# Performance work log

Measured on AMD Instinct MI355X. Metric: run time of the kernel, lower is better.

The kernel has to match this reference:

```python
import jax, jax.numpy as jnp
import numpy as np
from jax import lax

B, N = 8, 4096
H = 128          # cfg.net.num_hidden
K = 64           # max_num_neighbors
R1, R2 = 0.2, 0.4
S1, S2 = N // 2, N // 8   # sampling ratios 0.5 and 0.25
OUT = 40


def setup_inputs() -> dict:
    key = jax.random.key(0)
    ks = jax.random.split(key, 32)
    inp = {}
    inp["x"] = jax.random.normal(ks[30], (B, N, 3), jnp.float32)
    inp["pos"] = jax.random.uniform(ks[31], (B, N, 3), jnp.float32)  # unit cube -> radii 0.2/0.4 meaningful
    layers = [("sa1_w1", "sa1_b1", 6, H // 2), ("sa1_w2", "sa1_b2", H // 2, H),
              ("sa2_w1", "sa2_b1", H + 3, H), ("sa2_w2", "sa2_b2", H, 2 * H),
              ("sa3_w1", "sa3_b1", 2 * H + 3, 2 * H), ("sa3_w2", "sa3_b2", 2 * H, 4 * H),
              ("sa3_w3", "sa3_b3", 4 * H, 8 * H),
              ("hd_w1", "hd_b1", 8 * H, 4 * H), ("hd_w2", "hd_b2", 4 * H, 2 * H),
              ("hd_w3", "hd_b3", 2 * H, OUT)]
    for i, (wn, bn, fi, fo) in enumerate(layers):
        inp[wn] = jax.random.normal(ks[i], (fi, fo), jnp.float32) / np.sqrt(fi)
        inp[bn] = jnp.zeros((fo,), jnp.float32)
    return inp


def _mlp(h, layers):
    # Linear+ReLU stack, plain last layer (PyG MLP plain_last=True, eval-mode BN is identity)
    n = len(layers)
    for i, (w, b) in enumerate(layers):
        h = h @ w + b
        if i < n - 1:
            h = jax.nn.relu(h)
    return h


def _fps(p, n_samples):
    # farthest point sampling on one cloud p: [N,3] -> [n_samples] int32
    Np = p.shape[0]

    def step(carry, _):
        min_d, last = carry
        d = jnp.sum((p - p[last]) ** 2, -1)
        min_d = jnp.minimum(min_d, d)
        return (min_d, jnp.argmax(min_d).astype(jnp.int32)), last

    _, idxs = lax.scan(step, (jnp.full((Np,), jnp.inf, p.dtype), jnp.int32(0)),
                       None, length=n_samples)
    return idxs


def _sa(xc, pc, n_samples, r, layers):
    # one SA layer on one cloud: xc [N,C], pc [N,3]
    idx = _fps(pc, n_samples)
    c = pc[idx]                                            # [S,3] centers
    d2 = jnp.sum((c[:, None, :] - pc[None, :, :]) ** 2, -1)  # [S,N]
    d2 = jnp.where(d2 <= r * r, d2, jnp.inf)               # ball query mask
    negd, nbr = lax.top_k(-d2, K)                          # K nearest inside ball
    valid = jnp.isfinite(negd)                             # [S,K]
    feat = jnp.concatenate([xc[nbr], pc[nbr] - c[:, None, :]], -1)  # [S,K,C+3]
    h = _mlp(feat, layers)                                 # [S,K,Cout]
    h = jnp.where(valid[..., None], h, -jnp.inf)
    return jnp.max(h, axis=1), c                           # max-pool over neighborhood


def reference(x, pos, sa1_w1, sa1_b1, sa1_w2, sa1_b2,
              sa2_w1, sa2_b1, sa2_w2, sa2_b2,
              sa3_w1, sa3_b1, sa3_w2, sa3_b2, sa3_w3, sa3_b3,
              hd_w1, hd_b1, hd_w2, hd_b2, hd_w3, hd_b3):
    x1, p1 = jax.vmap(lambda xc, pc: _sa(xc, pc, S1, R1,
                                         [(sa1_w1, sa1_b1), (sa1_w2, sa1_b2)]))(x, pos)
    x2, p2 = jax.vmap(lambda xc, pc: _sa(xc, pc, S2, R2,
                                         [(sa2_w1, sa2_b1), (sa2_w2, sa2_b2)]))(x1, p1)
    # GlobalSAModule: MLP(cat([x,pos])) then global max pool over remaining points
    g = _mlp(jnp.concatenate([x2, p2], -1),
             [(sa3_w1, sa3_b1), (sa3_w2, sa3_b2), (sa3_w3, sa3_b3)])
    g = jnp.max(g, axis=1)                                 # [B, 8H]
    # head MLP (dropout inactive at eval)
    return _mlp(g, [(hd_w1, hd_b1), (hd_w2, hd_b2), (hd_w3, hd_b3)])
```

## Files before the change

kernel.cpp:

```cpp
#include <hip/hip_runtime.h>


constexpr int NBATCH = 8;

template<int CTRL>
__device__ __forceinline__ float dpp_max_step(float v) {
  int o = __builtin_amdgcn_update_dpp(__float_as_int(v), __float_as_int(v),
                                      CTRL, 0xf, 0xf, false);
  return fmaxf(v, __int_as_float(o));
}
__device__ __forceinline__ float wave_max_bcast(float v) {
  v = dpp_max_step<0x111>(v);
  v = dpp_max_step<0x112>(v);
  v = dpp_max_step<0x114>(v);
  v = dpp_max_step<0x118>(v);
  v = dpp_max_step<0x142>(v);
  v = dpp_max_step<0x143>(v);
  return __int_as_float(__builtin_amdgcn_readlane(__float_as_int(v), 63));
}
template<int CTRL>
__device__ __forceinline__ int dpp_add_step(int v) {
  int o = __builtin_amdgcn_update_dpp(0, v, CTRL, 0xf, 0xf, true);
  return v + o;
}
__device__ __forceinline__ int wave_sum_bcast(int v) {
  v = dpp_add_step<0x111>(v);
  v = dpp_add_step<0x112>(v);
  v = dpp_add_step<0x114>(v);
  v = dpp_add_step<0x118>(v);
  v = dpp_add_step<0x142>(v);
  v = dpp_add_step<0x143>(v);
  return __builtin_amdgcn_readlane(v, 63);
}

template<int NPTS, int NTH>
__global__ __launch_bounds__(NTH) void fps_kernel(const float* __restrict__ pos,
    int nsamp, int* __restrict__ idx_out, float* __restrict__ c_out) {
#pragma clang fp contract(off)
  constexpr int PT = NPTS / NTH;
  constexpr int NW = NTH / 64;
  const int b = blockIdx.x;
  const float* p = pos + (size_t)b * NPTS * 3;
  int* idxb = idx_out + (size_t)b * nsamp;
  float* cb = c_out + (size_t)b * nsamp * 3;
  __shared__ float lx[NPTS], ly[NPTS], lz[NPTS];
  __shared__ unsigned long long wkey[2][NW];
  const int t = threadIdx.x, lane = t & 63, w = t >> 6;
  float px[PT], py[PT], pz[PT], md[PT];
#pragma unroll
  for (int i = 0; i < PT; i++) {
    int j = t * PT + i;
    px[i] = p[j * 3 + 0]; py[i] = p[j * 3 + 1]; pz[i] = p[j * 3 + 2];
    lx[j] = px[i]; ly[j] = py[i]; lz[j] = pz[i];
    md[i] = __builtin_inff();
  }
  __syncthreads();
  int cur = 0;
  for (int s = 0;; ++s) {
    float cx = lx[cur], cy = ly[cur], cz = lz[cur];
    if (t == 0) { idxb[s] = cur; cb[s * 3 + 0] = cx; cb[s * 3 + 1] = cy; cb[s * 3 + 2] = cz; }
    if (s == nsamp - 1) break;
    float bv = -__builtin_inff(); int bi = 0;
#pragma unroll
    for (int i = 0; i < PT; i++) {
      float dx = px[i] - cx, dy = py[i] - cy, dz = pz[i] - cz;
      float d = (dx * dx + dy * dy) + dz * dz;
      float m = fminf(md[i], d); md[i] = m;
      if (m > bv) { bv = m; bi = i; }
    }
    float wmax = wave_max_bcast(bv);
    unsigned long long ball = __ballot(bv == wmax);
    int fl = __ffsll((long long)ball) - 1;
    int ib = __builtin_amdgcn_readlane(bi, fl);
    int gidx = ((w << 6) + fl) * PT + ib;
    if (lane == 0)
      wkey[s & 1][w] = (((unsigned long long)(unsigned)__float_as_int(wmax)) << 32)
                       | (unsigned)(~gidx);
    __syncthreads();
    unsigned long long best = wkey[s & 1][0];
#pragma unroll
    for (int q = 1; q < NW; q++) {
      unsigned long long k2 = wkey[s & 1][q];
      if (k2 > best) best = k2;
    }
    cur = (int)(~(unsigned)best);
  }
}

template<int NPTS, int SPB>
__global__ __launch_bounds__(256) void ballquery_kernel(const float* __restrict__ pts,
    const float* __restrict__ ctr, float rr,
    int* __restrict__ nbr, int* __restrict__ cnt_out) {
#pragma clang fp contract(off)
  const int gw = (blockIdx.x << 2) + (threadIdx.x >> 6);
  const int lane = threadIdx.x & 63;
  const int b = gw / SPB;
  __shared__ unsigned long long list_[4][1024];
  unsigned long long* list = list_[threadIdx.x >> 6];
  const float* p = pts + (size_t)b * NPTS * 3;
  const float* c = ctr + (size_t)gw * 3;
  const float cx = c[0], cy = c[1], cz = c[2];
  const unsigned long long lmask = (1ull << lane) - 1ull;
  int cnt = 0;
  for (int j0 = 0; j0 < NPTS; j0 += 64) {
    int j = j0 + lane;
    float dx = p[j * 3 + 0] - cx, dy = p[j * 3 + 1] - cy, dz = p[j * 3 + 2] - cz;
    float d = (dx * dx + dy * dy) + dz * dz;
    bool in = (d <= rr);
    unsigned long long bal = __ballot(in);
    int pos = cnt + __popcll(bal & lmask);
    if (in && pos < 1024)
      list[pos] = (((unsigned long long)__float_as_uint(d)) << 32) | (unsigned)j;
    cnt += __popcll(bal);
  }
  if (cnt > 1024) cnt = 1024;
  __syncthreads();
  int* nbrp = nbr + (size_t)gw * 64;
  const int nr = (cnt + 63) >> 6;
  unsigned long long key[16];
#pragma unroll
  for (int r = 0; r < 16; r++) {
    int slot = r * 64 + lane;
    key[r] = (r < nr && slot < cnt) ? list[slot] : ~0ull;
  }
  if (cnt <= 64) {
    nbrp[lane] = (lane < cnt) ? (int)(unsigned)key[0] : 0;
    if (lane == 0) cnt_out[gw] = cnt;
    return;
  }
  unsigned pref = 0; int cbase = 0;
  for (int bit = 29; bit >= 0; --bit) {
    int cc = 0;
#pragma unroll
    for (int r = 0; r < 16; r++) if (r < nr) {
      unsigned db = (unsigned)(key[r] >> 32);
      cc += ((db >> bit) == (pref >> bit)) ? 1 : 0;
    }
    cc = wave_sum_bcast(cc);
    if (cbase + cc < 64) { cbase += cc; pref |= (1u << bit); }
  }
  int base = 0;
#pragma unroll
  for (int r = 0; r < 16; r++) if (r < nr) {
    unsigned db = (unsigned)(key[r] >> 32);
    bool sel = db < pref;
    unsigned long long m = __ballot(sel);
    if (sel) nbrp[base + __popcll(m & lmask)] = (int)(unsigned)key[r];
    base += __popcll(m);
  }
  int need = 64 - base;
  for (int t2 = 0; t2 < need; ++t2) {
    unsigned besti = 0xffffffffu;
#pragma unroll
    for (int r = 0; r < 16; r++) if (r < nr) {
      if ((unsigned)(key[r] >> 32) == pref) {
        unsigned v = (unsigned)key[r];
        besti = v < besti ? v : besti;
      }
    }
#pragma unroll
    for (int off = 32; off; off >>= 1) {
      unsigned o = __shfl_xor(besti, off, 64);
      besti = o < besti ? o : besti;
    }
    unsigned long long wk = (((unsigned long long)pref) << 32) | besti;
#pragma unroll
    for (int r = 0; r < 16; r++) if (r < nr && key[r] == wk) key[r] = ~0ull;
    if (lane == 0) nbrp[base + t2] = (int)besti;
  }
  if (lane == 0) cnt_out[gw] = 64;
}

__global__ __launch_bounds__(256) void q1_kernel(const float* __restrict__ x,
    const float* __restrict__ pos, const float* __restrict__ w, float* __restrict__ q) {
  int gw = (blockIdx.x << 2) + (threadIdx.x >> 6), lane = threadIdx.x & 63;
  const float* xr = x + (size_t)gw * 3; const float* pr = pos + (size_t)gw * 3;
  float a = 0.f;
#pragma unroll
  for (int m = 0; m < 3; m++) a = fmaf(xr[m], w[m * 64 + lane], a);
#pragma unroll
  for (int m = 0; m < 3; m++) a = fmaf(pr[m], w[(3 + m) * 64 + lane], a);
  q[(size_t)gw * 64 + lane] = a;
}

__global__ __launch_bounds__(256) void t1_kernel(const float* __restrict__ c1,
    const float* __restrict__ w, const float* __restrict__ b1, float* __restrict__ t) {
  int gw = (blockIdx.x << 2) + (threadIdx.x >> 6), lane = threadIdx.x & 63;
  const float* cr = c1 + (size_t)gw * 3;
  float a = b1[lane];
#pragma unroll
  for (int m = 0; m < 3; m++) a = fmaf(-cr[m], w[(3 + m) * 64 + lane], a);
  t[(size_t)gw * 64 + lane] = a;
}

__global__ __launch_bounds__(256) void q2_kernel(const float* __restrict__ x1,
    const float* __restrict__ p1, const float* __restrict__ w, float* __restrict__ q2) {
  int gw = (blockIdx.x << 2) + (threadIdx.x >> 6), lane = threadIdx.x & 63;
  const float* xr = x1 + (size_t)gw * 128; const float* pr = p1 + (size_t)gw * 3;
  float a0 = 0.f, a1 = 0.f;
#pragma unroll 8
  for (int m = 0; m < 128; m++) {
    float v = xr[m];
    a0 = fmaf(v, w[m * 128 + lane], a0);
    a1 = fmaf(v, w[m * 128 + 64 + lane], a1);
  }
#pragma unroll
  for (int m = 0; m < 3; m++) {
    float v = pr[m];
    a0 = fmaf(v, w[(128 + m) * 128 + lane], a0);
    a1 = fmaf(v, w[(128 + m) * 128 + 64 + lane], a1);
  }
  q2[(size_t)gw * 128 + lane] = a0;
  q2[(size_t)gw * 128 + 64 + lane] = a1;
}

__global__ __launch_bounds__(256) void t2_kernel(const float* __restrict__ c2,
    const float* __restrict__ w, const float* __restrict__ b1, float* __restrict__ t) {
  int gw = (blockIdx.x << 2) + (threadIdx.x >> 6), lane = threadIdx.x & 63;
  const float* cr = c2 + (size_t)gw * 3;
  float a0 = b1[lane], a1 = b1[64 + lane];
#pragma unroll
  for (int m = 0; m < 3; m++) {
    a0 = fmaf(-cr[m], w[(128 + m) * 128 + lane], a0);
    a1 = fmaf(-cr[m], w[(128 + m) * 128 + 64 + lane], a1);
  }
  t[(size_t)gw * 128 + lane] = a0;
  t[(size_t)gw * 128 + 64 + lane] = a1;
}

template<int CIN, int COUT, int OSTR, int NPB, int SPB>
__global__ __launch_bounds__(256) void sa_pool(const float* __restrict__ q,
    const float* __restrict__ t, const int* __restrict__ nbr, const int* __restrict__ cnt,
    const float* __restrict__ w2, const float* __restrict__ b2, float* __restrict__ out) {
  int gw = (blockIdx.x << 2) + (threadIdx.x >> 6), lane = threadIdx.x & 63;
  int b = gw / SPB;
  int nk = nbr[(size_t)gw * 64 + lane];
  int c = cnt[gw];
  const float* qr = q + ((size_t)b * NPB + nk) * CIN;
  const float* tr = t + (size_t)gw * CIN;
  float h[CIN];
#pragma unroll
  for (int i = 0; i < CIN; i += 4) {
    float4 v = *(const float4*)(qr + i);
    h[i]     = fmaxf(v.x + tr[i], 0.f);
    h[i + 1] = fmaxf(v.y + tr[i + 1], 0.f);
    h[i + 2] = fmaxf(v.z + tr[i + 2], 0.f);
    h[i + 3] = fmaxf(v.w + tr[i + 3], 0.f);
  }
  bool valid = lane < c;
  float* op = out + (size_t)gw * OSTR;
#pragma unroll 1
  for (int nc = 0; nc < COUT; nc += 16) {
    float acc[16];
#pragma unroll
    for (int u = 0; u < 16; u++) acc[u] = b2[nc + u];
#pragma unroll
    for (int i = 0; i < CIN; i++) {
      const float* wr = w2 + (size_t)i * COUT + nc;
#pragma unroll
      for (int u = 0; u < 16; u++) acc[u] = fmaf(h[i], wr[u], acc[u]);
    }
#pragma unroll
    for (int u = 0; u < 16; u++) {
      float v = valid ? acc[u] : -__builtin_inff();
#pragma unroll
      for (int off = 32; off; off >>= 1) v = fmaxf(v, __shfl_xor(v, off, 64));
      acc[u] = v;
    }
    if (lane == 0) {
#pragma unroll
      for (int u = 0; u < 16; u += 4)
        *(float4*)(op + nc + u) = make_float4(acc[u], acc[u + 1], acc[u + 2], acc[u + 3]);
    }
  }
}

__global__ void concat3_kernel(const float* __restrict__ c2, float* __restrict__ xin3) {
  int row = blockIdx.x * 256 + threadIdx.x;
  if (row < NBATCH * 512) {
    float* o = xin3 + (size_t)row * 272 + 256;
    const float* c = c2 + (size_t)row * 3;
    o[0] = c[0]; o[1] = c[1]; o[2] = c[2];
#pragma unroll
    for (int i = 3; i < 16; i++) o[i] = 0.f;
  }
}

template<int K, int KP, int N, int AST, bool RELU>
__global__ __launch_bounds__(256) void gemm64(const float* __restrict__ A,
    const float* __restrict__ W, const float* __restrict__ bias, float* __restrict__ C) {
  constexpr int NT = N / 64;
  const int bid = blockIdx.x, tid = threadIdx.x;
  const int tm = bid / NT, tn = bid % NT;
  __shared__ __align__(16) float As[16][68];
  __shared__ __align__(16) float Ws[16][68];
  const int arow = tid >> 2, acol = (tid & 3) << 2;
  const int wrow = tid >> 4, wcol = (tid & 15) << 2;
  const int ty = tid >> 4, tx = tid & 15;
  const float* Ap = A + (size_t)(tm * 64 + arow) * AST + acol;
  const float* Wp = W + (size_t)tn * 64 + wcol;
  float acc[4][4] = {};
  for (int k0 = 0; k0 < KP; k0 += 16) {
    float4 av = *(const float4*)(Ap + k0);
    As[acol + 0][arow] = av.x; As[acol + 1][arow] = av.y;
    As[acol + 2][arow] = av.z; As[acol + 3][arow] = av.w;
    int krow = k0 + wrow;
    float4 wv = make_float4(0.f, 0.f, 0.f, 0.f);
    if (krow < K) wv = *(const float4*)(Wp + (size_t)krow * N);
    *(float4*)(&Ws[wrow][wcol]) = wv;
    __syncthreads();
#pragma unroll
    for (int kk = 0; kk < 16; kk++) {
      float4 a4 = *(const float4*)(&As[kk][ty << 2]);
      float4 b4 = *(const float4*)(&Ws[kk][tx << 2]);
      float aa[4] = {a4.x, a4.y, a4.z, a4.w};
      float bb[4] = {b4.x, b4.y, b4.z, b4.w};
#pragma unroll
      for (int mm = 0; mm < 4; mm++)
#pragma unroll
        for (int nn = 0; nn < 4; nn++) acc[mm][nn] = fmaf(aa[mm], bb[nn], acc[mm][nn]);
    }
    __syncthreads();
  }
  const int m0 = tm * 64 + (ty << 2), n0 = tn * 64 + (tx << 2);
#pragma unroll
  for (int mm = 0; mm < 4; mm++) {
    float4 o;
    o.x = acc[mm][0] + bias[n0 + 0];
    o.y = acc[mm][1] + bias[n0 + 1];
    o.z = acc[mm][2] + bias[n0 + 2];
    o.w = acc[mm][3] + bias[n0 + 3];
    if (RELU) { o.x = fmaxf(o.x, 0.f); o.y = fmaxf(o.y, 0.f);
                o.z = fmaxf(o.z, 0.f); o.w = fmaxf(o.w, 0.f); }
    *(float4*)(C + (size_t)(m0 + mm) * N + n0) = o;
  }
}

__global__ void gmax_kernel(const float* __restrict__ h, float* __restrict__ g) {
  int n = blockIdx.x * 256 + threadIdx.x;
  int b = n >> 10, col = n & 1023;
  const float* p = h + ((size_t)b * 512) * 1024 + col;
  float m = -__builtin_inff();
  for (int j = 0; j < 512; j++) m = fmaxf(m, p[(size_t)j * 1024]);
  g[n] = m;
}

__global__ __launch_bounds__(256) void head_kernel(const float* __restrict__ g,
    const float* __restrict__ w1, const float* __restrict__ b1,
    const float* __restrict__ w2, const float* __restrict__ b2,
    const float* __restrict__ w3, const float* __restrict__ b3,
    float* __restrict__ out) {
  int b = blockIdx.x, t = threadIdx.x;
  __shared__ float s1[1024];
  __shared__ float s2[512];
  *(float4*)(s1 + t * 4) = *(const float4*)(g + (size_t)b * 1024 + t * 4);
  __syncthreads();
  {
    float a0 = b1[t], a1 = b1[t + 256];
    for (int i = 0; i < 1024; i++) {
      float v = s1[i];
      a0 = fmaf(v, w1[(size_t)i * 512 + t], a0);
      a1 = fmaf(v, w1[(size_t)i * 512 + t + 256], a1);
    }
    s2[t] = fmaxf(a0, 0.f); s2[t + 256] = fmaxf(a1, 0.f);
  }
  __syncthreads();
  {
    float a = b2[t];
    for (int i = 0; i < 512; i++) a = fmaf(s2[i], w2[(size_t)i * 256 + t], a);
    s1[t] = fmaxf(a, 0.f);
  }
  __syncthreads();
  if (t < 40) {
    float a = b3[t];
    for (int i = 0; i < 256; i++) a = fmaf(s1[i], w3[(size_t)i * 40 + t], a);
    out[(size_t)b * 40 + t] = a;
  }
}

extern "C" void kernel_launch(void* const* d_in, const int* in_sizes, int n_in,
                              void* d_out, int out_size, void* d_ws, size_t ws_size,
                              hipStream_t stream) {
  const float* x   = (const float*)d_in[0];
  const float* pos = (const float*)d_in[1];
  const float* w11 = (const float*)d_in[2];  const float* b11 = (const float*)d_in[3];
  const float* w12 = (const float*)d_in[4];  const float* b12 = (const float*)d_in[5];
  const float* w21 = (const float*)d_in[6];  const float* b21 = (const float*)d_in[7];
  const float* w22 = (const float*)d_in[8];  const float* b22 = (const float*)d_in[9];
  const float* w31 = (const float*)d_in[10]; const float* b31 = (const float*)d_in[11];
  const float* w32 = (const float*)d_in[12]; const float* b32 = (const float*)d_in[13];
  const float* w33 = (const float*)d_in[14]; const float* b33 = (const float*)d_in[15];
  const float* hw1 = (const float*)d_in[16]; const float* hb1 = (const float*)d_in[17];
  const float* hw2 = (const float*)d_in[18]; const float* hb2 = (const float*)d_in[19];
  const float* hw3 = (const float*)d_in[20]; const float* hb3 = (const float*)d_in[21];
  float* out = (float*)d_out;

  char* wsb = (char*)d_ws;
  int*   idx1 = (int*)(wsb + 0);
  int*   idx2 = (int*)(wsb + 65536);
  int*   cnt1 = (int*)(wsb + 81920);
  int*   cnt2 = (int*)(wsb + 147456);
  float* c1   = (float*)(wsb + 163840);
  float* c2   = (float*)(wsb + 360448);
  float* g    = (float*)(wsb + 409600);
  char* big = wsb + 524288;
  int*   nbr1 = (int*)(big + 0);
  float* q1   = (float*)(big + 4194304);
  float* t1   = (float*)(big + 12582912);
  float* h3c  = (float*)(big + 0);
  float* x1   = (float*)(big + 16777216);
  int*   nbr2 = (int*)(big + 25165824);
  float* h3b  = (float*)(big + 16777216);
  float* q2   = (float*)(big + 26214400);
  float* h3a  = (float*)(big + 26214400);
  float* t2   = (float*)(big + 34603008);
  float* xin3 = (float*)(big + 36700160);

  const float RR1 = (float)(0.2 * 0.2);
  const float RR2 = (float)(0.4 * 0.4);

  fps_kernel<4096, 512><<<NBATCH, 512, 0, stream>>>(pos, 2048, idx1, c1);
  q1_kernel<<<8192, 256, 0, stream>>>(x, pos, w11, q1);
  t1_kernel<<<4096, 256, 0, stream>>>(c1, w11, b11, t1);
  ballquery_kernel<4096, 2048><<<4096, 256, 0, stream>>>(pos, c1, RR1, nbr1, cnt1);
  sa_pool<64, 128, 128, 4096, 2048><<<4096, 256, 0, stream>>>(q1, t1, nbr1, cnt1, w12, b12, x1);
  fps_kernel<2048, 512><<<NBATCH, 512, 0, stream>>>(c1, 512, idx2, c2);
  q2_kernel<<<4096, 256, 0, stream>>>(x1, c1, w21, q2);
  t2_kernel<<<1024, 256, 0, stream>>>(c2, w21, b21, t2);
  ballquery_kernel<2048, 512><<<1024, 256, 0, stream>>>(c1, c2, RR2, nbr2, cnt2);
  sa_pool<128, 256, 272, 2048, 512><<<1024, 256, 0, stream>>>(q2, t2, nbr2, cnt2, w22, b22, xin3);
  concat3_kernel<<<16, 256, 0, stream>>>(c2, xin3);
  gemm64<259, 272, 256, 272, true ><<<256,  256, 0, stream>>>(xin3, w31, b31, h3a);
  gemm64<256, 256, 512, 256, true ><<<512,  256, 0, stream>>>(h3a,  w32, b32, h3b);
  gemm64<512, 512, 1024, 512, false><<<1024, 256, 0, stream>>>(h3b, w33, b33, h3c);
  gmax_kernel<<<32, 256, 0, stream>>>(h3c, g);
  head_kernel<<<NBATCH, 256, 0, stream>>>(g, hw1, hb1, hw2, hb2, hw3, hb3, out);

  (void)in_sizes; (void)n_in; (void)out_size; (void)ws_size;
}
```

Measured before the change: 3.577 ms.

## Carry winning point coords through FPS reduction and pack distance math

The FPS kernel no longer stages all points in LDS and reads the next center from shared memory after each step. Each wave now broadcasts its winner's coordinates alongside the key, so the block-level reduction picks up the new center directly. This removes a dependent LDS load from the serial loop. Distance math uses 2-wide float vectors, which can map to packed FP32 ops. The block size drops from 512 to 256 threads, which means fewer waves to reduce across but more points held in registers per thread.

```diff
diff --git a/kernel.cpp b/kernel.cpp
--- a/kernel.cpp
+++ b/kernel.cpp
@@ -2,6 +2,8 @@
 
 
 constexpr int NBATCH = 8;
+
+typedef float v2f __attribute__((ext_vector_type(2)));
 
 template<int CTRL>
 __device__ __forceinline__ float dpp_max_step(float v) {
@@ -38,52 +40,76 @@
     int nsamp, int* __restrict__ idx_out, float* __restrict__ c_out) {
 #pragma clang fp contract(off)
   constexpr int PT = NPTS / NTH;
+  constexpr int NP = PT / 2;
   constexpr int NW = NTH / 64;
   const int b = blockIdx.x;
   const float* p = pos + (size_t)b * NPTS * 3;
   int* idxb = idx_out + (size_t)b * nsamp;
   float* cb = c_out + (size_t)b * nsamp * 3;
-  __shared__ float lx[NPTS], ly[NPTS], lz[NPTS];
-  __shared__ unsigned long long wkey[2][NW];
+  __shared__ unsigned long long skey[2][NW];
+  __shared__ float sxyz[2][NW][3];
   const int t = threadIdx.x, lane = t & 63, w = t >> 6;
-  float px[PT], py[PT], pz[PT], md[PT];
-#pragma unroll
-  for (int i = 0; i < PT; i++) {
-    int j = t * PT + i;
-    px[i] = p[j * 3 + 0]; py[i] = p[j * 3 + 1]; pz[i] = p[j * 3 + 2];
-    lx[j] = px[i]; ly[j] = py[i]; lz[j] = pz[i];
-    md[i] = __builtin_inff();
-  }
-  __syncthreads();
+  v2f px[NP], py[NP], pz[NP], md[NP];
+#pragma unroll
+  for (int k = 0; k < NP; k++) {
+    int j = t * PT + 2 * k;
+    px[k] = (v2f){p[j * 3 + 0], p[j * 3 + 3]};
+    py[k] = (v2f){p[j * 3 + 1], p[j * 3 + 4]};
+    pz[k] = (v2f){p[j * 3 + 2], p[j * 3 + 5]};
+    md[k] = (v2f){__builtin_inff(), __builtin_inff()};
+  }
+  float cx = p[0], cy = p[1], cz = p[2];
   int cur = 0;
   for (int s = 0;; ++s) {
-    float cx = lx[cur], cy = ly[cur], cz = lz[cur];
     if (t == 0) { idxb[s] = cur; cb[s * 3 + 0] = cx; cb[s * 3 + 1] = cy; cb[s * 3 + 2] = cz; }
     if (s == nsamp - 1) break;
     float bv = -__builtin_inff(); int bi = 0;
-#pragma unroll
-    for (int i = 0; i < PT; i++) {
-      float dx = px[i] - cx, dy = py[i] - cy, dz = pz[i] - cz;
-      float d = (dx * dx + dy * dy) + dz * dz;
-      float m = fminf(md[i], d); md[i] = m;
-      if (m > bv) { bv = m; bi = i; }
+    v2f cxv = {cx, cx}, cyv = {cy, cy}, czv = {cz, cz};
+#pragma unroll
+    for (int k = 0; k < NP; k++) {
+      v2f dx = px[k] - cxv, dy = py[k] - cyv, dz = pz[k] - czv;
+      v2f d = (dx * dx + dy * dy) + dz * dz;
+      v2f m;
+      m.x = fminf(md[k].x, d.x); m.y = fminf(md[k].y, d.y);
+      md[k] = m;
+      if (m.x > bv) { bv = m.x; bi = 2 * k; }
+      if (m.y > bv) { bv = m.y; bi = 2 * k + 1; }
     }
     float wmax = wave_max_bcast(bv);
     unsigned long long ball = __ballot(bv == wmax);
     int fl = __ffsll((long long)ball) - 1;
     int ib = __builtin_amdgcn_readlane(bi, fl);
     int gidx = ((w << 6) + fl) * PT + ib;
-    if (lane == 0)
-      wkey[s & 1][w] = (((unsigned long long)(unsigned)__float_as_int(wmax)) << 32)
+    int kk = ib >> 1;
+    v2f sx = px[0], sy = py[0], sz = pz[0];
+#pragma unroll
+    for (int k = 1; k < NP; k++)
+      if (kk == k) { sx = px[k]; sy = py[k]; sz = pz[k]; }
+    float wx = (ib & 1) ? sx.y : sx.x;
+    float wy = (ib & 1) ? sy.y : sy.x;
+    float wz = (ib & 1) ? sz.y : sz.x;
+    wx = __int_as_float(__builtin_amdgcn_readlane(__float_as_int(wx), fl));
+    wy = __int_as_float(__builtin_amdgcn_readlane(__float_as_int(wy), fl));
+    wz = __int_as_float(__builtin_amdgcn_readlane(__float_as_int(wz), fl));
+    if (lane == 0) {
+      skey[s & 1][w] = (((unsigned long long)(unsigned)__float_as_int(wmax)) << 32)
                        | (unsigned)(~gidx);
+      sxyz[s & 1][w][0] = wx; sxyz[s & 1][w][1] = wy; sxyz[s & 1][w][2] = wz;
+    }
     __syncthreads();
-    unsigned long long best = wkey[s & 1][0];
+    unsigned long long best = skey[s & 1][0];
+    float nx = sxyz[s & 1][0][0], ny = sxyz[s & 1][0][1], nz = sxyz[s & 1][0][2];
 #pragma unroll
     for (int q = 1; q < NW; q++) {
-      unsigned long long k2 = wkey[s & 1][q];
-      if (k2 > best) best = k2;
+      unsigned long long k2 = skey[s & 1][q];
+      bool gt = k2 > best;
+      best = gt ? k2 : best;
+      nx = gt ? sxyz[s & 1][q][0] : nx;
+      ny = gt ? sxyz[s & 1][q][1] : ny;
+      nz = gt ? sxyz[s & 1][q][2] : nz;
     }
     cur = (int)(~(unsigned)best);
+    cx = nx; cy = ny; cz = nz;
   }
 }
 
@@ -419,12 +445,12 @@
   const float RR1 = (float)(0.2 * 0.2);
   const float RR2 = (float)(0.4 * 0.4);
 
-  fps_kernel<4096, 512><<<NBATCH, 512, 0, stream>>>(pos, 2048, idx1, c1);
+  fps_kernel<4096, 256><<<NBATCH, 256, 0, stream>>>(pos, 2048, idx1, c1);
   q1_kernel<<<8192, 256, 0, stream>>>(x, pos, w11, q1);
   t1_kernel<<<4096, 256, 0, stream>>>(c1, w11, b11, t1);
   ballquery_kernel<4096, 2048><<<4096, 256, 0, stream>>>(pos, c1, RR1, nbr1, cnt1);
   sa_pool<64, 128, 128, 4096, 2048><<<4096, 256, 0, stream>>>(q1, t1, nbr1, cnt1, w12, b12, x1);
-  fps_kernel<2048, 512><<<NBATCH, 512, 0, stream>>>(c1, 512, idx2, c2);
+  fps_kernel<2048, 256><<<NBATCH, 256, 0, stream>>>(c1, 512, idx2, c2);
   q2_kernel<<<4096, 256, 0, stream>>>(x1, c1, w21, q2);
   t2_kernel<<<1024, 256, 0, stream>>>(c2, w21, b21, t2);
   ballquery_kernel<2048, 512><<<1024, 256, 0, stream>>>(c1, c2, RR2, nbr2, cnt2);
```

Result: slower. 4.385 ms (+22.6%).

## Overlap serial FPS kernels with independent work via fused multi-role launches

Applied to the files above, without the earlier changes.

Merges independent stages into shared launches so the long single-block-per-batch FPS runs beside the work that does not depend on it. Stage-1 FPS runs with the q1 projection, stage-2 FPS (moved earlier) runs with ball query 1 and t1, and SA1 pooling runs with ball query 2, t2 and the concat step. FPS now writes centers from shared memory after the loop instead of thread 0 writing them each step. Risks: fused kernels share the largest shared-memory and register footprint across roles, and fuse1 uses 512-thread blocks, so q1 now indexes 8 waves per block.

```diff
diff --git a/kernel.cpp b/kernel.cpp
--- a/kernel.cpp
+++ b/kernel.cpp
@@ -33,18 +33,14 @@
   return __builtin_amdgcn_readlane(v, 63);
 }
 
-template<int NPTS, int NTH>
-__global__ __launch_bounds__(NTH) void fps_kernel(const float* __restrict__ pos,
-    int nsamp, int* __restrict__ idx_out, float* __restrict__ c_out) {
+template<int NPTS, int NTH, int NSAMP>
+__device__ void fps_body(const float* __restrict__ p, float* __restrict__ cb) {
 #pragma clang fp contract(off)
   constexpr int PT = NPTS / NTH;
   constexpr int NW = NTH / 64;
-  const int b = blockIdx.x;
-  const float* p = pos + (size_t)b * NPTS * 3;
-  int* idxb = idx_out + (size_t)b * nsamp;
-  float* cb = c_out + (size_t)b * nsamp * 3;
   __shared__ float lx[NPTS], ly[NPTS], lz[NPTS];
   __shared__ unsigned long long wkey[2][NW];
+  __shared__ int sidx[NSAMP];
   const int t = threadIdx.x, lane = t & 63, w = t >> 6;
   float px[PT], py[PT], pz[PT], md[PT];
 #pragma unroll
@@ -58,8 +54,8 @@
   int cur = 0;
   for (int s = 0;; ++s) {
     float cx = lx[cur], cy = ly[cur], cz = lz[cur];
-    if (t == 0) { idxb[s] = cur; cb[s * 3 + 0] = cx; cb[s * 3 + 1] = cy; cb[s * 3 + 2] = cz; }
-    if (s == nsamp - 1) break;
+    if (t == 0) sidx[s] = cur;
+    if (s == NSAMP - 1) break;
     float bv = -__builtin_inff(); int bi = 0;
 #pragma unroll
     for (int i = 0; i < PT; i++) {
@@ -85,14 +81,19 @@
     }
     cur = (int)(~(unsigned)best);
   }
+  __syncthreads();
+  for (int i = t; i < NSAMP; i += NTH) {
+    int id = sidx[i];
+    cb[i * 3 + 0] = lx[id]; cb[i * 3 + 1] = ly[id]; cb[i * 3 + 2] = lz[id];
+  }
 }
 
 template<int NPTS, int SPB>
-__global__ __launch_bounds__(256) void ballquery_kernel(const float* __restrict__ pts,
+__device__ void ballquery_body(int bb, const float* __restrict__ pts,
     const float* __restrict__ ctr, float rr,
     int* __restrict__ nbr, int* __restrict__ cnt_out) {
 #pragma clang fp contract(off)
-  const int gw = (blockIdx.x << 2) + (threadIdx.x >> 6);
+  const int gw = (bb << 2) + (threadIdx.x >> 6);
   const int lane = threadIdx.x & 63;
   const int b = gw / SPB;
   __shared__ unsigned long long list_[4][1024];
@@ -171,9 +172,9 @@
   if (lane == 0) cnt_out[gw] = 64;
 }
 
-__global__ __launch_bounds__(256) void q1_kernel(const float* __restrict__ x,
+__device__ void q1_body(int bb, const float* __restrict__ x,
     const float* __restrict__ pos, const float* __restrict__ w, float* __restrict__ q) {
-  int gw = (blockIdx.x << 2) + (threadIdx.x >> 6), lane = threadIdx.x & 63;
+  int gw = bb * 8 + (threadIdx.x >> 6), lane = threadIdx.x & 63;
   const float* xr = x + (size_t)gw * 3; const float* pr = pos + (size_t)gw * 3;
   float a = 0.f;
 #pragma unroll
@@ -183,14 +184,127 @@
   q[(size_t)gw * 64 + lane] = a;
 }
 
-__global__ __launch_bounds__(256) void t1_kernel(const float* __restrict__ c1,
+__device__ void t1_body(int bb, const float* __restrict__ c1,
     const float* __restrict__ w, const float* __restrict__ b1, float* __restrict__ t) {
-  int gw = (blockIdx.x << 2) + (threadIdx.x >> 6), lane = threadIdx.x & 63;
+  int gw = (bb << 2) + (threadIdx.x >> 6), lane = threadIdx.x & 63;
   const float* cr = c1 + (size_t)gw * 3;
   float a = b1[lane];
 #pragma unroll
   for (int m = 0; m < 3; m++) a = fmaf(-cr[m], w[(3 + m) * 64 + lane], a);
   t[(size_t)gw * 64 + lane] = a;
+}
+
+__device__ void t2_body(int bb, const float* __restrict__ c2,
+    const float* __restrict__ w, const float* __restrict__ b1, float* __restrict__ t) {
+  int gw = (bb << 2) + (threadIdx.x >> 6), lane = threadIdx.x & 63;
+  const float* cr = c2 + (size_t)gw * 3;
+  float a0 = b1[lane], a1 = b1[64 + lane];
+#pragma unroll
+  for (int m = 0; m < 3; m++) {
+    a0 = fmaf(-cr[m], w[(128 + m) * 128 + lane], a0);
+    a1 = fmaf(-cr[m], w[(128 + m) * 128 + 64 + lane], a1);
+  }
+  t[(size_t)gw * 128 + lane] = a0;
+  t[(size_t)gw * 128 + 64 + lane] = a1;
+}
+
+__device__ void concat3_body(int bb, const float* __restrict__ c2, float* __restrict__ xin3) {
+  int row = bb * 256 + threadIdx.x;
+  if (row < NBATCH * 512) {
+    float* o = xin3 + (size_t)row * 272 + 256;
+    const float* c = c2 + (size_t)row * 3;
+    o[0] = c[0]; o[1] = c[1]; o[2] = c[2];
+#pragma unroll
+    for (int i = 3; i < 16; i++) o[i] = 0.f;
+  }
+}
+
+template<int CIN, int COUT, int OSTR, int NPB, int SPB>
+__device__ void sa_pool_body(int bb, const float* __restrict__ q,
+    const float* __restrict__ t, const int* __restrict__ nbr, const int* __restrict__ cnt,
+    const float* __restrict__ w2, const float* __restrict__ b2, float* __restrict__ out) {
+  int gw = (bb << 2) + (threadIdx.x >> 6), lane = threadIdx.x & 63;
+  int b = gw / SPB;
+  int nk = nbr[(size_t)gw * 64 + lane];
+  int c = cnt[gw];
+  const float* qr = q + ((size_t)b * NPB + nk) * CIN;
+  const float* tr = t + (size_t)gw * CIN;
+  float h[CIN];
+#pragma unroll
+  for (int i = 0; i < CIN; i += 4) {
+    float4 v = *(const float4*)(qr + i);
+    h[i]     = fmaxf(v.x + tr[i], 0.f);
+    h[i + 1] = fmaxf(v.y + tr[i + 1], 0.f);
+    h[i + 2] = fmaxf(v.z + tr[i + 2], 0.f);
+    h[i + 3] = fmaxf(v.w + tr[i + 3], 0.f);
+  }
+  bool valid = lane < c;
+  float* op = out + (size_t)gw * OSTR;
+#pragma unroll 1
+  for (int nc = 0; nc < COUT; nc += 16) {
+    float acc[16];
+#pragma unroll
+    for (int u = 0; u < 16; u++) acc[u] = b2[nc + u];
+#pragma unroll
+    for (int i = 0; i < CIN; i++) {
+      const float* wr = w2 + (size_t)i * COUT + nc;
+#pragma unroll
+      for (int u = 0; u < 16; u++) acc[u] = fmaf(h[i], wr[u], acc[u]);
+    }
+#pragma unroll
+    for (int u = 0; u < 16; u++) {
+      float v = valid ? acc[u] : -__builtin_inff();
+#pragma unroll
+      for (int off = 32; off; off >>= 1) v = fmaxf(v, __shfl_xor(v, off, 64));
+      acc[u] = v;
+    }
+    if (lane == 0) {
+#pragma unroll
+      for (int u = 0; u < 16; u += 4)
+        *(float4*)(op + nc + u) = make_float4(acc[u], acc[u + 1], acc[u + 2], acc[u + 3]);
+    }
+  }
+}
+
+__global__ __launch_bounds__(512) void fuse1_kernel(const float* __restrict__ pos,
+    const float* __restrict__ x, const float* __restrict__ w11,
+    float* __restrict__ c1, float* __restrict__ q1) {
+  int bid = blockIdx.x;
+  if (bid < 8)
+    fps_body<4096, 512, 2048>(pos + (size_t)bid * 4096 * 3, c1 + (size_t)bid * 2048 * 3);
+  else
+    q1_body(bid - 8, x, pos, w11, q1);
+}
+
+__global__ __launch_bounds__(256) void fuse2_kernel(const float* __restrict__ pos,
+    const float* __restrict__ c1, const float* __restrict__ w11, const float* __restrict__ b11,
+    float* __restrict__ c2, int* __restrict__ nbr1, int* __restrict__ cnt1,
+    float* __restrict__ t1buf, float rr1) {
+  int bid = blockIdx.x;
+  if (bid < 8)
+    fps_body<2048, 256, 512>(c1 + (size_t)bid * 2048 * 3, c2 + (size_t)bid * 512 * 3);
+  else if (bid < 8 + 4096)
+    ballquery_body<4096, 2048>(bid - 8, pos, c1, rr1, nbr1, cnt1);
+  else
+    t1_body(bid - (8 + 4096), c1, w11, b11, t1buf);
+}
+
+__global__ __launch_bounds__(256) void fuse3_kernel(const float* __restrict__ q1buf,
+    const float* __restrict__ t1buf, const int* __restrict__ nbr1, const int* __restrict__ cnt1,
+    const float* __restrict__ w12, const float* __restrict__ b12, float* __restrict__ x1,
+    const float* __restrict__ c1, const float* __restrict__ c2, float rr2,
+    int* __restrict__ nbr2, int* __restrict__ cnt2,
+    const float* __restrict__ w21, const float* __restrict__ b21, float* __restrict__ t2buf,
+    float* __restrict__ xin3) {
+  int bid = blockIdx.x;
+  if (bid < 4096)
+    sa_pool_body<64, 128, 128, 4096, 2048>(bid, q1buf, t1buf, nbr1, cnt1, w12, b12, x1);
+  else if (bid < 4096 + 1024)
+    ballquery_body<2048, 512>(bid - 4096, c1, c2, rr2, nbr2, cnt2);
+  else if (bid < 4096 + 1024 + 1024)
+    t2_body(bid - (4096 + 1024), c2, w21, b21, t2buf);
+  else
+    concat3_body(bid - (4096 + 1024 + 1024), c2, xin3);
 }
 
 __global__ __launch_bounds__(256) void q2_kernel(const float* __restrict__ x1,
@@ -214,76 +328,10 @@
   q2[(size_t)gw * 128 + 64 + lane] = a1;
 }
 
-__global__ __launch_bounds__(256) void t2_kernel(const float* __restrict__ c2,
-    const float* __restrict__ w, const float* __restrict__ b1, float* __restrict__ t) {
-  int gw = (blockIdx.x << 2) + (threadIdx.x >> 6), lane = threadIdx.x & 63;
-  const float* cr = c2 + (size_t)gw * 3;
-  float a0 = b1[lane], a1 = b1[64 + lane];
-#pragma unroll
-  for (int m = 0; m < 3; m++) {
-    a0 = fmaf(-cr[m], w[(128 + m) * 128 + lane], a0);
-    a1 = fmaf(-cr[m], w[(128 + m) * 128 + 64 + lane], a1);
-  }
-  t[(size_t)gw * 128 + lane] = a0;
-  t[(size_t)gw * 128 + 64 + lane] = a1;
-}
-
-template<int CIN, int COUT, int OSTR, int NPB, int SPB>
-__global__ __launch_bounds__(256) void sa_pool(const float* __restrict__ q,
+__global__ __launch_bounds__(256) void sa_pool2_kernel(const float* __restrict__ q,
     const float* __restrict__ t, const int* __restrict__ nbr, const int* __restrict__ cnt,
     const float* __restrict__ w2, const float* __restrict__ b2, float* __restrict__ out) {
-  int gw = (blockIdx.x << 2) + (threadIdx.x >> 6), lane = threadIdx.x & 63;
-  int b = gw / SPB;
-  int nk = nbr[(size_t)gw * 64 + lane];
-  int c = cnt[gw];
-  const float* qr = q + ((size_t)b * NPB + nk) * CIN;
-  const float* tr = t + (size_t)gw * CIN;
-  float h[CIN];
-#pragma unroll
-  for (int i = 0; i < CIN; i += 4) {
-    float4 v = *(const float4*)(qr + i);
-    h[i]     = fmaxf(v.x + tr[i], 0.f);
-    h[i + 1] = fmaxf(v.y + tr[i + 1], 0.f);
-    h[i + 2] = fmaxf(v.z + tr[i + 2], 0.f);
-    h[i + 3] = fmaxf(v.w + tr[i + 3], 0.f);
-  }
-  bool valid = lane < c;
-  float* op = out + (size_t)gw * OSTR;
-#pragma unroll 1
-  for (int nc = 0; nc < COUT; nc += 16) {
-    float acc[16];
-#pragma unroll
-    for (int u = 0; u < 16; u++) acc[u] = b2[nc + u];
-#pragma unroll
-    for (int i = 0; i < CIN; i++) {
-      const float* wr = w2 + (size_t)i * COUT + nc;
-#pragma unroll
-      for (int u = 0; u < 16; u++) acc[u] = fmaf(h[i], wr[u], acc[u]);
-    }
-#pragma unroll
-    for (int u = 0; u < 16; u++) {
-      float v = valid ? acc[u] : -__builtin_inff();
-#pragma unroll
-      for (int off = 32; off; off >>= 1) v = fmaxf(v, __shfl_xor(v, off, 64));
-      acc[u] = v;
-    }
-    if (lane == 0) {
-#pragma unroll
-      for (int u = 0; u < 16; u += 4)
-        *(float4*)(op + nc + u) = make_float4(acc[u], acc[u + 1], acc[u + 2], acc[u + 3]);
-    }
-  }
-}
-
-__global__ void concat3_kernel(const float* __restrict__ c2, float* __restrict__ xin3) {
-  int row = blockIdx.x * 256 + threadIdx.x;
-  if (row < NBATCH * 512) {
-    float* o = xin3 + (size_t)row * 272 + 256;
-    const float* c = c2 + (size_t)row * 3;
-    o[0] = c[0]; o[1] = c[1]; o[2] = c[2];
-#pragma unroll
-    for (int i = 3; i < 16; i++) o[i] = 0.f;
-  }
+  sa_pool_body<128, 256, 272, 2048, 512>(blockIdx.x, q, t, nbr, cnt, w2, b2, out);
 }
 
 template<int K, int KP, int N, int AST, bool RELU>
@@ -396,8 +444,6 @@
   float* out = (float*)d_out;
 
   char* wsb = (char*)d_ws;
-  int*   idx1 = (int*)(wsb + 0);
-  int*   idx2 = (int*)(wsb + 65536);
   int*   cnt1 = (int*)(wsb + 81920);
   int*   cnt2 = (int*)(wsb + 147456);
   float* c1   = (float*)(wsb + 163840);
@@ -419,17 +465,13 @@
   const float RR1 = (float)(0.2 * 0.2);
   const float RR2 = (float)(0.4 * 0.4);
 
-  fps_kernel<4096, 512><<<NBATCH, 512, 0, stream>>>(pos, 2048, idx1, c1);
-  q1_kernel<<<8192, 256, 0, stream>>>(x, pos, w11, q1);
-  t1_kernel<<<4096, 256, 0, stream>>>(c1, w11, b11, t1);
-  ballquery_kernel<4096, 2048><<<4096, 256, 0, stream>>>(pos, c1, RR1, nbr1, cnt1);
-  sa_pool<64, 128, 128, 4096, 2048><<<4096, 256, 0, stream>>>(q1, t1, nbr1, cnt1, w12, b12, x1);
-  fps_kernel<2048, 512><<<NBATCH, 512, 0, stream>>>(c1, 512, idx2, c2);
+  fuse1_kernel<<<8 + 4096, 512, 0, stream>>>(pos, x, w11, c1, q1);
+  fuse2_kernel<<<8 + 4096 + 4096, 256, 0, stream>>>(pos, c1, w11, b11,
+                                                    c2, nbr1, cnt1, t1, RR1);
+  fuse3_kernel<<<4096 + 1024 + 1024 + 16, 256, 0, stream>>>(q1, t1, nbr1, cnt1,
+      w12, b12, x1, c1, c2, RR2, nbr2, cnt2, w21, b21, t2, xin3);
   q2_kernel<<<4096, 256, 0, stream>>>(x1, c1, w21, q2);
-  t2_kernel<<<1024, 256, 0, stream>>>(c2, w21, b21, t2);
-  ballquery_kernel<2048, 512><<<1024, 256, 0, stream>>>(c1, c2, RR2, nbr2, cnt2);
-  sa_pool<128, 256, 272, 2048, 512><<<1024, 256, 0, stream>>>(q2, t2, nbr2, cnt2, w22, b22, xin3);
-  concat3_kernel<<<16, 256, 0, stream>>>(c2, xin3);
+  sa_pool2_kernel<<<1024, 256, 0, stream>>>(q2, t2, nbr2, cnt2, w22, b22, xin3);
   gemm64<259, 272, 256, 272, true ><<<256,  256, 0, stream>>>(xin3, w31, b31, h3a);
   gemm64<256, 256, 512, 256, true ><<<512,  256, 0, stream>>>(h3a,  w32, b32, h3b);
   gemm64<512, 512, 1024, 512, false><<<1024, 256, 0, stream>>>(h3b, w33, b33, h3c);
```

New measurement: 3.535 ms. About the same (-1.2%).
